# Kernel tuning notes

Hardware: AMD Instinct MI355X
Metric: run time of the kernel (lower is better)

Reference implementation:

```python
import jax, jax.numpy as jnp
import numpy as np

B, T, S, E, H = 4, 32, 256, 512, 8
D = E // H
SCALE = np.sqrt(D).astype(np.float32)
Q_MOD, K_MOD = 0, 1


def setup_inputs() -> dict:
    key = jax.random.key(0)
    ks = jax.random.split(key, 12)
    def spikes(k):
        return (jax.random.uniform(k, (B, T, S, E)) < 0.1).astype(jnp.float32)
    init = lambda k, shp: jax.random.normal(k, shp, dtype=jnp.float32) * (1.0 / np.sqrt(shp[0]))
    return {
        "query_spikes": spikes(ks[0]),
        "key_spikes": spikes(ks[1]),
        "value_spikes": spikes(ks[2]),
        "Wq": init(ks[3], (E, E)), "bq": jnp.zeros((E,), jnp.float32),
        "Wk": init(ks[4], (E, E)), "bk": jnp.zeros((E,), jnp.float32),
        "Wv": init(ks[5], (E, E)), "bv": jnp.zeros((E,), jnp.float32),
        "Wo": init(ks[6], (E, E)), "bo": jnp.zeros((E,), jnp.float32),
        "modality_weights": jnp.ones((2, H), jnp.float32),          # nn.Parameter(torch.ones(2, num_heads))
        "temporal_sync": jax.random.normal(ks[7], (T, H), jnp.float32) * 0.1,  # torch.randn(T, H) * 0.1
    }


def _spike_softmax(scores):
    # sigmoid((s - max)*5) normalized along key axis
    m = jnp.max(scores, axis=-1, keepdims=True)
    p = jax.nn.sigmoid((scores - m) * 5.0)
    return p / (jnp.sum(p, axis=-1, keepdims=True) + 1e-8)


def reference(query_spikes, key_spikes, value_spikes, Wq, bq, Wk, bk, Wv, bv, Wo, bo,
              modality_weights, temporal_sync):
    def proj(x, W, b):  # [B,T,S,E] -> [B,T,H,S,D]
        y = jnp.einsum("btse,ef->btsf", x, W) + b
        return y.reshape(B, T, S, H, D).transpose(0, 1, 3, 2, 4)

    Q = proj(query_spikes, Wq, bq)
    K = proj(key_spikes, Wk, bk)
    V = proj(value_spikes, Wv, bv)

    # attention scores across all timesteps at once: [B,T,H,Sq,Sk]
    scores = jnp.einsum("bthqd,bthkd->bthqk", Q, K) / SCALE
    mod_w = (modality_weights[Q_MOD] * modality_weights[K_MOD]).reshape(1, 1, H, 1, 1)
    scores = scores * mod_w + temporal_sync.reshape(1, T, H, 1, 1)

    attn = _spike_softmax(scores)
    attended = jnp.einsum("bthqk,bthkd->bthqd", attn, V)   # [B,T,H,Sq,D]
    attended = attended.transpose(0, 1, 3, 2, 4).reshape(B, T, S, E)
    return jnp.einsum("btse,ef->btsf", attended, Wo) + bo
```

## Files before the change

### kernel.cpp

```cpp
#include <hip/hip_runtime.h>
#include <hip/hip_bf16.h>

#define DI __device__ __forceinline__

typedef __bf16 bf16x8 __attribute__((ext_vector_type(8)));
typedef float  f32x4  __attribute__((ext_vector_type(4)));
typedef float  f32x16 __attribute__((ext_vector_type(16)));


DI ushort f2bf(float f) {
  union { float f; unsigned u; } v; v.f = f;
  unsigned r = v.u + 0x7fffu + ((v.u >> 16) & 1u);
  return (ushort)(r >> 16);
}

DI unsigned cvtpk2(float a, float b) {
  unsigned r;
  asm("v_cvt_pk_bf16_f32 %0, %1, %2" : "=v"(r) : "v"(a), "v"(b));
  return r;
}

DI float rcpf(float x) {
  float r;
  asm("v_rcp_f32 %0, %1" : "=v"(r) : "v"(x));
  return r;
}

DI void gload_lds16(const void* g, void* lds) {
  __builtin_amdgcn_global_load_lds(
      (const __attribute__((address_space(1))) unsigned*)g,
      (__attribute__((address_space(3))) unsigned*)lds, 16, 0, 0);
}

DI f32x4 zero4() { f32x4 z; z[0] = 0.f; z[1] = 0.f; z[2] = 0.f; z[3] = 0.f; return z; }

DI f32x16 zero16() {
  f32x16 z;
  for (int i = 0; i < 16; i++) z[i] = 0.f;
  return z;
}

union BF8U { ushort u[8]; unsigned d[4]; bf16x8 v; };

__global__ __launch_bounds__(256) void wtrans_kernel(
    const float* __restrict__ W0, const float* __restrict__ W1,
    const float* __restrict__ W2, const float* __restrict__ W3,
    ushort* __restrict__ out) {
  __shared__ float tile[64][65];
  const float* W = blockIdx.z == 0 ? W0 : blockIdx.z == 1 ? W1 : blockIdx.z == 2 ? W2 : W3;
  ushort* o = out + (size_t)blockIdx.z * 512 * 512;
  int k0 = blockIdx.x * 64, n0 = blockIdx.y * 64;
  int tid = threadIdx.x;
#pragma unroll
  for (int i = 0; i < 16; i++) {
    int idx = i * 256 + tid; int r = idx >> 6, c = idx & 63;
    tile[r][c] = W[(size_t)(k0 + r) * 512 + n0 + c];
  }
  __syncthreads();
#pragma unroll
  for (int i = 0; i < 16; i++) {
    int idx = i * 256 + tid; int r = idx >> 6, c = idx & 63;
    o[(size_t)(n0 + r) * 512 + k0 + c] = f2bf(tile[c][r]);
  }
}

template <int AF32>
DI void gemm_core(const void* Ap, const ushort* __restrict__ Bt, int m0, int n0,
                  char* Alds, char* Blds, f32x4 (&acc)[4][4]) {
  const float*  Af = (const float*)Ap;
  const ushort* Ah = (const ushort*)Ap;
  int tid = threadIdx.x, lane = tid & 63, wv = tid >> 6;
  int wm = (wv >> 1) * 64, wn = (wv & 1) * 64;
  int srow = tid >> 3, skg = tid & 7;

  float4 ar[8];
  bf16x8 ab[4];

  auto issueB = [&](int t) {
    char* Bb = Blds + (t & 1) * 16384;
#pragma unroll
    for (int i = 0; i < 4; i++) {
      int c = (wv * 4 + i) * 64 + lane;
      int r = c >> 3, g = (c & 7) ^ (r & 7);
      gload_lds16(Bt + (size_t)(n0 + r) * 512 + t * 64 + g * 8, Bb + (wv * 4 + i) * 1024);
    }
  };
  auto loadA = [&](int t) {
    if (AF32) {
#pragma unroll
      for (int rr = 0; rr < 4; rr++) {
        const float4* p = (const float4*)(Af + (size_t)(m0 + srow + rr * 32) * 512 + t * 64 + skg * 8);
        ar[rr * 2] = p[0]; ar[rr * 2 + 1] = p[1];
      }
    } else {
#pragma unroll
      for (int rr = 0; rr < 4; rr++)
        ab[rr] = *(const bf16x8*)(Ah + (size_t)(m0 + srow + rr * 32) * 512 + t * 64 + skg * 8);
    }
  };
  auto writeA = [&]() {
#pragma unroll
    for (int rr = 0; rr < 4; rr++) {
      int r = srow + rr * 32;
      BF8U av;
      if (AF32) {
        av.d[0] = cvtpk2(ar[rr * 2].x, ar[rr * 2].y);
        av.d[1] = cvtpk2(ar[rr * 2].z, ar[rr * 2].w);
        av.d[2] = cvtpk2(ar[rr * 2 + 1].x, ar[rr * 2 + 1].y);
        av.d[3] = cvtpk2(ar[rr * 2 + 1].z, ar[rr * 2 + 1].w);
      } else {
        av.v = ab[rr];
      }
      *(bf16x8*)(Alds + ((r * 128 + skg * 16) ^ ((r & 7) << 4))) = av.v;
    }
  };
  auto compute = [&](int t) {
    char* Bb = Blds + (t & 1) * 16384;
#pragma unroll
    for (int ks = 0; ks < 2; ks++) {
      bf16x8 a[4], b[4];
#pragma unroll
      for (int i = 0; i < 4; i++) {
        int ra = wm + i * 16 + (lane & 15);
        a[i] = *(const bf16x8*)(Alds + ((ra * 128 + (ks * 4 + (lane >> 4)) * 16) ^ ((ra & 7) << 4)));
        int rb = wn + i * 16 + (lane & 15);
        b[i] = *(const bf16x8*)(Bb + ((rb * 128 + (ks * 4 + (lane >> 4)) * 16) ^ ((rb & 7) << 4)));
      }
#pragma unroll
      for (int i = 0; i < 4; i++)
#pragma unroll
        for (int j = 0; j < 4; j++)
          acc[i][j] = __builtin_amdgcn_mfma_f32_16x16x32_bf16(a[i], b[j], acc[i][j], 0, 0, 0);
    }
  };

  issueB(0); loadA(0); writeA();
  __syncthreads();

#pragma unroll
  for (int t = 0; t < 8; t++) {
    if (t < 7) { issueB(t + 1); loadA(t + 1); }
    compute(t);
    __syncthreads();
    if (t < 7) writeA();
    __syncthreads();
  }
}

__global__ __launch_bounds__(256, 3) void qkv_gemm_kernel(
    const float* __restrict__ Aq, const float* __restrict__ Ak, const float* __restrict__ Av,
    const ushort* __restrict__ Wt, const float* __restrict__ bqp,
    const float* __restrict__ bkp, const float* __restrict__ bvp,
    ushort* __restrict__ Qw, ushort* __restrict__ Kw, ushort* __restrict__ Vt) {
  __shared__ __align__(16) char Alds[16384];
  __shared__ __align__(16) char Blds[32768];
  int z = blockIdx.z;
  const float* A = z == 0 ? Aq : z == 1 ? Ak : Av;
  const ushort* Bt = Wt + (size_t)z * 262144;
  const float* bias = z == 0 ? bqp : z == 1 ? bkp : bvp;
  int bl = ((int)blockIdx.x & 7) * 128 + ((int)blockIdx.x >> 3);
  int m0 = (bl >> 2) * 128, n0 = (bl & 3) * 128;

  f32x4 acc[4][4];
#pragma unroll
  for (int i = 0; i < 4; i++)
#pragma unroll
    for (int j = 0; j < 4; j++) acc[i][j] = zero4();

  gemm_core<1>(A, Bt, m0, n0, Alds, Blds, acc);

  int lane = threadIdx.x & 63, wv = threadIdx.x >> 6;
  int wm = (wv >> 1) * 64, wn = (wv & 1) * 64;
#pragma unroll
  for (int j = 0; j < 4; j++) {
    int col = n0 + wn + j * 16 + (lane & 15);
    float bv = bias[col];
#pragma unroll
    for (int i = 0; i < 4; i++) {
      int row0 = m0 + wm + i * 16 + (lane >> 4) * 4;
      if (z == 2) {
        int btv = row0 >> 8, s = row0 & 255;
        ushort4 w;
        w.x = f2bf(acc[i][j][0] + bv); w.y = f2bf(acc[i][j][1] + bv);
        w.z = f2bf(acc[i][j][2] + bv); w.w = f2bf(acc[i][j][3] + bv);
        *(ushort4*)(Vt + ((size_t)btv * 512 + col) * 256 + s) = w;
      } else {
        ushort* C = z == 0 ? Qw : Kw;
#pragma unroll
        for (int r = 0; r < 4; r++)
          C[(size_t)(row0 + r) * 512 + col] = f2bf(acc[i][j][r] + bv);
      }
    }
  }
}

__global__ __launch_bounds__(256, 3) void out_gemm_kernel(
    const ushort* __restrict__ A, const ushort* __restrict__ Bt,
    const float* __restrict__ bias, float* __restrict__ C) {
  __shared__ __align__(16) char Alds[16384];
  __shared__ __align__(16) char Blds[32768];
  int bl = ((int)blockIdx.x & 7) * 128 + ((int)blockIdx.x >> 3);
  int m0 = (bl >> 2) * 128, n0 = (bl & 3) * 128;

  f32x4 acc[4][4];
#pragma unroll
  for (int i = 0; i < 4; i++)
#pragma unroll
    for (int j = 0; j < 4; j++) acc[i][j] = zero4();

  gemm_core<0>(A, Bt, m0, n0, Alds, Blds, acc);

  int lane = threadIdx.x & 63, wv = threadIdx.x >> 6;
  int wm = (wv >> 1) * 64, wn = (wv & 1) * 64;
#pragma unroll
  for (int j = 0; j < 4; j++) {
    int col = n0 + wn + j * 16 + (lane & 15);
    float bv = bias[col];
#pragma unroll
    for (int i = 0; i < 4; i++) {
      int row0 = m0 + wm + i * 16 + (lane >> 4) * 4;
#pragma unroll
      for (int r = 0; r < 4; r++)
        C[(size_t)(row0 + r) * 512 + col] = acc[i][j][r] + bv;
    }
  }
}

__global__ __launch_bounds__(256) void attn_kernel(
    const ushort* __restrict__ Q, const ushort* __restrict__ K,
    const ushort* __restrict__ Vt, const float* __restrict__ mw,
    ushort* __restrict__ att) {
  __shared__ __align__(16) char Klds[32768];
  __shared__ __align__(16) char Vlds[32768];
  int tid = threadIdx.x, lane = tid & 63, wv = tid >> 6;
  int lq = lane & 31, hi = lane >> 5;
  int b = blockIdx.x;
  int h = b & 7, bt = b >> 3;
  const ushort* Qb = Q + ((size_t)bt * 256 + wv * 64) * 512 + h * 64;
  const ushort* Kb = K + ((size_t)bt * 256) * 512 + h * 64;
  const ushort* Vb = Vt + ((size_t)bt * 512 + h * 64) * 256;
  float c0 = mw[h] * mw[8 + h] * 0.125f;

#pragma unroll
  for (int i = 0; i < 8; i++) {
    int ci = (wv * 8 + i) * 64 + lane;
    int l2 = ci & 31, h2 = (ci >> 5) & 1, ds = (ci >> 6) & 3, kt = ci >> 8;
    gload_lds16(Kb + (size_t)(kt * 32 + l2) * 512 + ds * 16 + h2 * 8,
                &Klds[(wv * 8 + i) * 1024]);
  }
  bf16x8 qf[2][4];
#pragma unroll
  for (int qj = 0; qj < 2; qj++)
#pragma unroll
    for (int ds = 0; ds < 4; ds++)
      qf[qj][ds] = *(const bf16x8*)(Qb + (size_t)(qj * 32 + lq) * 512 + ds * 16 + hi * 8);
  __syncthreads();

#pragma unroll
  for (int i = 0; i < 8; i++) {
    int ci = (wv * 8 + i) * 64 + lane;
    int l2 = ci & 31, h2 = (ci >> 5) & 1, df = (ci >> 6) & 1, ks = (ci >> 7) & 1, kt = ci >> 8;
    gload_lds16(Vb + (size_t)(df * 32 + l2) * 256 + kt * 32 + ks * 16 + h2 * 8,
                &Vlds[(wv * 8 + i) * 1024]);
  }

  float mx[2] = {-3.0e38f, -3.0e38f};
#pragma unroll 2
  for (int kt = 0; kt < 8; kt++) {
    bf16x8 kf[4];
#pragma unroll
    for (int ds = 0; ds < 4; ds++)
      kf[ds] = *(const bf16x8*)(&Klds[((kt * 4 + ds) * 2 + hi) * 512 + lq * 16]);
#pragma unroll
    for (int qj = 0; qj < 2; qj++) {
      f32x16 sT = zero16();
#pragma unroll
      for (int ds = 0; ds < 4; ds++)
        sT = __builtin_amdgcn_mfma_f32_32x32x16_bf16(kf[ds], qf[qj][ds], sT, 0, 0, 0);
#pragma unroll
      for (int r = 0; r < 16; r++) mx[qj] = fmaxf(mx[qj], sT[r] * c0);
    }
  }
#pragma unroll
  for (int qj = 0; qj < 2; qj++) mx[qj] = fmaxf(mx[qj], __shfl_xor(mx[qj], 32, 64));
  __syncthreads();

  float a5 = 5.f * c0;
  float m5[2] = {5.f * mx[0], 5.f * mx[1]};
  float sm[2] = {0.f, 0.f};
  f32x16 acc[2][2];
  acc[0][0] = zero16(); acc[0][1] = zero16(); acc[1][0] = zero16(); acc[1][1] = zero16();

#pragma unroll 2
  for (int kt = 0; kt < 8; kt++) {
    bf16x8 kf[4], vf[2][2];
#pragma unroll
    for (int ds = 0; ds < 4; ds++)
      kf[ds] = *(const bf16x8*)(&Klds[((kt * 4 + ds) * 2 + hi) * 512 + lq * 16]);
#pragma unroll
    for (int ks = 0; ks < 2; ks++)
#pragma unroll
      for (int df = 0; df < 2; df++)
        vf[ks][df] = *(const bf16x8*)(&Vlds[(((kt * 2 + ks) * 2 + df) * 2 + hi) * 512 + lq * 16]);
#pragma unroll
    for (int qj = 0; qj < 2; qj++) {
      f32x16 sT = zero16();
#pragma unroll
      for (int ds = 0; ds < 4; ds++)
        sT = __builtin_amdgcn_mfma_f32_32x32x16_bf16(kf[ds], qf[qj][ds], sT, 0, 0, 0);
      unsigned pk[8];
#pragma unroll
      for (int i = 0; i < 8; i++) {
        float p0 = rcpf(1.f + __expf(m5[qj] - sT[2 * i] * a5));
        float p1 = rcpf(1.f + __expf(m5[qj] - sT[2 * i + 1] * a5));
        sm[qj] += p0 + p1;
        pk[i] = cvtpk2(p0, p1);
      }
#pragma unroll
      for (int ks = 0; ks < 2; ks++) {
        int bb = ks * 4;
        unsigned sa = (unsigned)__shfl_xor((int)pk[bb + 0], 32, 64);
        unsigned sb = (unsigned)__shfl_xor((int)pk[bb + 1], 32, 64);
        unsigned sc = (unsigned)__shfl_xor((int)pk[bb + 2], 32, 64);
        unsigned sd = (unsigned)__shfl_xor((int)pk[bb + 3], 32, 64);
        BF8U pa;
        pa.d[0] = hi ? sc : pk[bb + 0];
        pa.d[1] = hi ? sd : pk[bb + 1];
        pa.d[2] = hi ? pk[bb + 2] : sa;
        pa.d[3] = hi ? pk[bb + 3] : sb;
#pragma unroll
        for (int df = 0; df < 2; df++)
          acc[qj][df] = __builtin_amdgcn_mfma_f32_32x32x16_bf16(pa.v, vf[ks][df], acc[qj][df], 0, 0, 0);
      }
    }
  }

#pragma unroll
  for (int qj = 0; qj < 2; qj++) sm[qj] += __shfl_xor(sm[qj], 32, 64);
  float rs[2] = {rcpf(sm[0] + 1e-8f), rcpf(sm[1] + 1e-8f)};
#pragma unroll
  for (int qj = 0; qj < 2; qj++) {
#pragma unroll
    for (int r = 0; r < 16; r++) {
      int ql = (r & 3) + 8 * (r >> 2) + 4 * hi;
      float rr = __shfl(rs[qj], ql, 64);
      size_t rowbase = ((size_t)bt * 256 + wv * 64 + qj * 32 + ql) * 512 + h * 64;
#pragma unroll
      for (int df = 0; df < 2; df++)
        att[rowbase + df * 32 + lq] = f2bf(acc[qj][df][r] * rr);
    }
  }
}

extern "C" void kernel_launch(void* const* d_in, const int* in_sizes, int n_in,
                              void* d_out, int out_size, void* d_ws, size_t ws_size,
                              hipStream_t stream) {
  (void)in_sizes; (void)n_in; (void)out_size; (void)ws_size;
  const float* qs  = (const float*)d_in[0];
  const float* ksn = (const float*)d_in[1];
  const float* vsn = (const float*)d_in[2];
  const float* Wq  = (const float*)d_in[3];
  const float* bq  = (const float*)d_in[4];
  const float* Wk  = (const float*)d_in[5];
  const float* bk  = (const float*)d_in[6];
  const float* Wv  = (const float*)d_in[7];
  const float* bv  = (const float*)d_in[8];
  const float* Wo  = (const float*)d_in[9];
  const float* bo  = (const float*)d_in[10];
  const float* mw  = (const float*)d_in[11];

  char* ws = (char*)d_ws;
  ushort* Wt = (ushort*)ws;
  ushort* Qw = (ushort*)(ws + (size_t)(2u << 20));
  ushort* Kw = (ushort*)(ws + (size_t)(2u << 20) + 33554432u);
  ushort* Vt = (ushort*)(ws + (size_t)(2u << 20) + 2u * 33554432u);
  ushort* Aw = (ushort*)(ws + (size_t)(2u << 20) + 3u * 33554432u);

  wtrans_kernel<<<dim3(8, 8, 4), 256, 0, stream>>>(Wq, Wk, Wv, Wo, Wt);
  qkv_gemm_kernel<<<dim3(1024, 1, 3), 256, 0, stream>>>(qs, ksn, vsn, Wt, bq, bk, bv,
                                                        Qw, Kw, Vt);
  attn_kernel<<<dim3(1024), 256, 0, stream>>>(Qw, Kw, Vt, mw, Aw);
  out_gemm_kernel<<<dim3(1024), 256, 0, stream>>>(Aw, Wt + 3 * 262144, bo, (float*)d_out);
}
```

Measured before the change: 212.2 us.

## Pre-convert spike inputs to bf16 and use async LDS-load pipelined GEMM

Adds a separate kernel that converts the fp32 spike inputs to bf16 in workspace, so both GEMMs can load A tiles directly into LDS with global_load_lds. The GEMM core becomes a double-buffered, prefetch-two-ahead pipeline with explicit vmcnt waits and barriers. This is meant to remove register staging and conversion from the GEMM inner loop. It adds an extra full read/write pass over the inputs and doubles LDS use, which lowers occupancy to two blocks per CU.

```diff
diff --git a/kernel.cpp b/kernel.cpp
--- a/kernel.cpp
+++ b/kernel.cpp
@@ -31,6 +31,11 @@
       (const __attribute__((address_space(1))) unsigned*)g,
       (__attribute__((address_space(3))) unsigned*)lds, 16, 0, 0);
 }
+
+#define WAITVM8   asm volatile("s_waitcnt vmcnt(8)" ::: "memory")
+#define WAITVM0   asm volatile("s_waitcnt vmcnt(0)" ::: "memory")
+#define WAITLGKM0 asm volatile("s_waitcnt lgkmcnt(0)" ::: "memory")
+#define SBAR      __builtin_amdgcn_s_barrier()
 
 DI f32x4 zero4() { f32x4 z; z[0] = 0.f; z[1] = 0.f; z[2] = 0.f; z[3] = 0.f; return z; }
 
@@ -64,57 +69,39 @@
   }
 }
 
-template <int AF32>
-DI void gemm_core(const void* Ap, const ushort* __restrict__ Bt, int m0, int n0,
-                  char* Alds, char* Blds, f32x4 (&acc)[4][4]) {
-  const float*  Af = (const float*)Ap;
-  const ushort* Ah = (const ushort*)Ap;
+__global__ __launch_bounds__(256) void cvt_kernel(
+    const float* __restrict__ q, const float* __restrict__ k,
+    const float* __restrict__ v, uint4* __restrict__ o) {
+  const float* src = blockIdx.y == 0 ? q : blockIdx.y == 1 ? k : v;
+  uint4* dst = o + (size_t)blockIdx.y * 2097152;
+  for (int i = blockIdx.x * 256 + threadIdx.x; i < 2097152; i += 2048 * 256) {
+    const float4* p = (const float4*)(src + (size_t)i * 8);
+    float4 a = p[0], b = p[1];
+    uint4 w;
+    w.x = cvtpk2(a.x, a.y); w.y = cvtpk2(a.z, a.w);
+    w.z = cvtpk2(b.x, b.y); w.w = cvtpk2(b.z, b.w);
+    dst[i] = w;
+  }
+}
+
+DI void gemm_core(const ushort* __restrict__ A, const ushort* __restrict__ Bt,
+                  int m0, int n0, char* Alds, char* Blds, f32x4 (&acc)[4][4]) {
   int tid = threadIdx.x, lane = tid & 63, wv = tid >> 6;
   int wm = (wv >> 1) * 64, wn = (wv & 1) * 64;
-  int srow = tid >> 3, skg = tid & 7;
-
-  float4 ar[8];
-  bf16x8 ab[4];
-
-  auto issueB = [&](int t) {
+
+  auto stage = [&](int t) {
+    char* Ab = Alds + (t & 1) * 16384;
     char* Bb = Blds + (t & 1) * 16384;
 #pragma unroll
     for (int i = 0; i < 4; i++) {
       int c = (wv * 4 + i) * 64 + lane;
       int r = c >> 3, g = (c & 7) ^ (r & 7);
+      gload_lds16(A + (size_t)(m0 + r) * 512 + t * 64 + g * 8, Ab + (wv * 4 + i) * 1024);
       gload_lds16(Bt + (size_t)(n0 + r) * 512 + t * 64 + g * 8, Bb + (wv * 4 + i) * 1024);
-    }
-  };
-  auto loadA = [&](int t) {
-    if (AF32) {
-#pragma unroll
-      for (int rr = 0; rr < 4; rr++) {
-        const float4* p = (const float4*)(Af + (size_t)(m0 + srow + rr * 32) * 512 + t * 64 + skg * 8);
-        ar[rr * 2] = p[0]; ar[rr * 2 + 1] = p[1];
-      }
-    } else {
-#pragma unroll
-      for (int rr = 0; rr < 4; rr++)
-        ab[rr] = *(const bf16x8*)(Ah + (size_t)(m0 + srow + rr * 32) * 512 + t * 64 + skg * 8);
-    }
-  };
-  auto writeA = [&]() {
-#pragma unroll
-    for (int rr = 0; rr < 4; rr++) {
-      int r = srow + rr * 32;
-      BF8U av;
-      if (AF32) {
-        av.d[0] = cvtpk2(ar[rr * 2].x, ar[rr * 2].y);
-        av.d[1] = cvtpk2(ar[rr * 2].z, ar[rr * 2].w);
-        av.d[2] = cvtpk2(ar[rr * 2 + 1].x, ar[rr * 2 + 1].y);
-        av.d[3] = cvtpk2(ar[rr * 2 + 1].z, ar[rr * 2 + 1].w);
-      } else {
-        av.v = ab[rr];
-      }
-      *(bf16x8*)(Alds + ((r * 128 + skg * 16) ^ ((r & 7) << 4))) = av.v;
     }
   };
   auto compute = [&](int t) {
+    char* Ab = Alds + (t & 1) * 16384;
     char* Bb = Blds + (t & 1) * 16384;
 #pragma unroll
     for (int ks = 0; ks < 2; ks++) {
@@ -122,7 +109,7 @@
 #pragma unroll
       for (int i = 0; i < 4; i++) {
         int ra = wm + i * 16 + (lane & 15);
-        a[i] = *(const bf16x8*)(Alds + ((ra * 128 + (ks * 4 + (lane >> 4)) * 16) ^ ((ra & 7) << 4)));
+        a[i] = *(const bf16x8*)(Ab + ((ra * 128 + (ks * 4 + (lane >> 4)) * 16) ^ ((ra & 7) << 4)));
         int rb = wn + i * 16 + (lane & 15);
         b[i] = *(const bf16x8*)(Bb + ((rb * 128 + (ks * 4 + (lane >> 4)) * 16) ^ ((rb & 7) << 4)));
       }
@@ -134,28 +121,28 @@
     }
   };
 
-  issueB(0); loadA(0); writeA();
-  __syncthreads();
-
+  stage(0);
+  stage(1);
 #pragma unroll
   for (int t = 0; t < 8; t++) {
-    if (t < 7) { issueB(t + 1); loadA(t + 1); }
+    if (t < 7) WAITVM8; else WAITVM0;
+    SBAR;
     compute(t);
-    __syncthreads();
-    if (t < 7) writeA();
-    __syncthreads();
-  }
-}
-
-__global__ __launch_bounds__(256, 3) void qkv_gemm_kernel(
-    const float* __restrict__ Aq, const float* __restrict__ Ak, const float* __restrict__ Av,
-    const ushort* __restrict__ Wt, const float* __restrict__ bqp,
-    const float* __restrict__ bkp, const float* __restrict__ bvp,
+    WAITLGKM0;
+    SBAR;
+    if (t < 6) stage(t + 2);
+  }
+}
+
+__global__ __launch_bounds__(256, 2) void qkv_gemm_kernel(
+    const ushort* __restrict__ Asp, const ushort* __restrict__ Wt,
+    const float* __restrict__ bqp, const float* __restrict__ bkp,
+    const float* __restrict__ bvp,
     ushort* __restrict__ Qw, ushort* __restrict__ Kw, ushort* __restrict__ Vt) {
-  __shared__ __align__(16) char Alds[16384];
+  __shared__ __align__(16) char Alds[32768];
   __shared__ __align__(16) char Blds[32768];
   int z = blockIdx.z;
-  const float* A = z == 0 ? Aq : z == 1 ? Ak : Av;
+  const ushort* A = Asp + (size_t)z * 16777216;
   const ushort* Bt = Wt + (size_t)z * 262144;
   const float* bias = z == 0 ? bqp : z == 1 ? bkp : bvp;
   int bl = ((int)blockIdx.x & 7) * 128 + ((int)blockIdx.x >> 3);
@@ -167,7 +154,7 @@
 #pragma unroll
     for (int j = 0; j < 4; j++) acc[i][j] = zero4();
 
-  gemm_core<1>(A, Bt, m0, n0, Alds, Blds, acc);
+  gemm_core(A, Bt, m0, n0, Alds, Blds, acc);
 
   int lane = threadIdx.x & 63, wv = threadIdx.x >> 6;
   int wm = (wv >> 1) * 64, wn = (wv & 1) * 64;
@@ -194,10 +181,10 @@
   }
 }
 
-__global__ __launch_bounds__(256, 3) void out_gemm_kernel(
+__global__ __launch_bounds__(256, 2) void out_gemm_kernel(
     const ushort* __restrict__ A, const ushort* __restrict__ Bt,
     const float* __restrict__ bias, float* __restrict__ C) {
-  __shared__ __align__(16) char Alds[16384];
+  __shared__ __align__(16) char Alds[32768];
   __shared__ __align__(16) char Blds[32768];
   int bl = ((int)blockIdx.x & 7) * 128 + ((int)blockIdx.x >> 3);
   int m0 = (bl >> 2) * 128, n0 = (bl & 3) * 128;
@@ -208,7 +195,7 @@
 #pragma unroll
     for (int j = 0; j < 4; j++) acc[i][j] = zero4();
 
-  gemm_core<0>(A, Bt, m0, n0, Alds, Blds, acc);
+  gemm_core(A, Bt, m0, n0, Alds, Blds, acc);
 
   int lane = threadIdx.x & 63, wv = threadIdx.x >> 6;
   int wm = (wv >> 1) * 64, wn = (wv & 1) * 64;
@@ -370,15 +357,18 @@
   const float* mw  = (const float*)d_in[11];
 
   char* ws = (char*)d_ws;
-  ushort* Wt = (ushort*)ws;
-  ushort* Qw = (ushort*)(ws + (size_t)(2u << 20));
-  ushort* Kw = (ushort*)(ws + (size_t)(2u << 20) + 33554432u);
-  ushort* Vt = (ushort*)(ws + (size_t)(2u << 20) + 2u * 33554432u);
-  ushort* Aw = (ushort*)(ws + (size_t)(2u << 20) + 3u * 33554432u);
+  const size_t SLOT = 33554432u;
+  ushort* Wt  = (ushort*)ws;
+  char*   s0  = ws + (size_t)(2u << 20);
+  ushort* Qw  = (ushort*)(s0 + 0 * SLOT);
+  ushort* Kw  = (ushort*)(s0 + 1 * SLOT);
+  ushort* Vt  = (ushort*)(s0 + 2 * SLOT);
+  ushort* Asp = (ushort*)(s0 + 3 * SLOT);
+  ushort* Aw  = (ushort*)(s0 + 3 * SLOT);
 
   wtrans_kernel<<<dim3(8, 8, 4), 256, 0, stream>>>(Wq, Wk, Wv, Wo, Wt);
-  qkv_gemm_kernel<<<dim3(1024, 1, 3), 256, 0, stream>>>(qs, ksn, vsn, Wt, bq, bk, bv,
-                                                        Qw, Kw, Vt);
+  cvt_kernel<<<dim3(2048, 3), 256, 0, stream>>>(qs, ksn, vsn, (uint4*)Asp);
+  qkv_gemm_kernel<<<dim3(1024, 1, 3), 256, 0, stream>>>(Asp, Wt, bq, bk, bv, Qw, Kw, Vt);
   attn_kernel<<<dim3(1024), 256, 0, stream>>>(Qw, Kw, Vt, mw, Aw);
   out_gemm_kernel<<<dim3(1024), 256, 0, stream>>>(Aw, Wt + 3 * 262144, bo, (float*)d_out);
 }
```

Measured after the change: 236.4 us. 1.11x slower.

## Deepen GEMM software pipeline with double-buffered A and explicit waitcnt barriers

Applied to the files above, without the earlier changes.

Replaces the shared gemm_core with two specialised GEMM kernels. Each uses double-buffered A and B tiles in LDS, prefetches two k-steps ahead, and uses explicit s_waitcnt vmcnt/lgkmcnt with raw s_barrier, which cuts the two full __syncthreads per iteration down to finer-grained waits. The output GEMM now loads its bf16 A operand straight into LDS with global_load_lds instead of going through registers. LDS per block grows to 64KB and launch bounds drop from 3 to 2 blocks per CU, trading occupancy for deeper overlap; the hand-counted vmcnt values are fragile if the number of loads changes.

```diff
diff --git a/kernel.cpp b/kernel.cpp
--- a/kernel.cpp
+++ b/kernel.cpp
@@ -31,6 +31,12 @@
       (const __attribute__((address_space(1))) unsigned*)g,
       (__attribute__((address_space(3))) unsigned*)lds, 16, 0, 0);
 }
+
+#define WAITVM12  asm volatile("s_waitcnt vmcnt(12)" ::: "memory")
+#define WAITVM8   asm volatile("s_waitcnt vmcnt(8)" ::: "memory")
+#define WAITVM0   asm volatile("s_waitcnt vmcnt(0)" ::: "memory")
+#define WAITLGKM0 asm volatile("s_waitcnt lgkmcnt(0)" ::: "memory")
+#define SBAR      __builtin_amdgcn_s_barrier()
 
 DI f32x4 zero4() { f32x4 z; z[0] = 0.f; z[1] = 0.f; z[2] = 0.f; z[3] = 0.f; return z; }
 
@@ -64,18 +70,51 @@
   }
 }
 
-template <int AF32>
-DI void gemm_core(const void* Ap, const ushort* __restrict__ Bt, int m0, int n0,
-                  char* Alds, char* Blds, f32x4 (&acc)[4][4]) {
-  const float*  Af = (const float*)Ap;
-  const ushort* Ah = (const ushort*)Ap;
+__global__ __launch_bounds__(256, 2) void qkv_gemm_kernel(
+    const float* __restrict__ Aq, const float* __restrict__ Ak, const float* __restrict__ Av,
+    const ushort* __restrict__ Wt, const float* __restrict__ bqp,
+    const float* __restrict__ bkp, const float* __restrict__ bvp,
+    ushort* __restrict__ Qw, ushort* __restrict__ Kw, ushort* __restrict__ Vt) {
+  __shared__ __align__(16) char Alds[32768];
+  __shared__ __align__(16) char Blds[32768];
+  int z = blockIdx.z;
+  const float* Af = z == 0 ? Aq : z == 1 ? Ak : Av;
+  const ushort* Bt = Wt + (size_t)z * 262144;
+  const float* bias = z == 0 ? bqp : z == 1 ? bkp : bvp;
+  int bl = ((int)blockIdx.x & 7) * 128 + ((int)blockIdx.x >> 3);
+  int m0 = (bl >> 2) * 128, n0 = (bl & 3) * 128;
   int tid = threadIdx.x, lane = tid & 63, wv = tid >> 6;
   int wm = (wv >> 1) * 64, wn = (wv & 1) * 64;
   int srow = tid >> 3, skg = tid & 7;
 
+  f32x4 acc[4][4];
+#pragma unroll
+  for (int i = 0; i < 4; i++)
+#pragma unroll
+    for (int j = 0; j < 4; j++) acc[i][j] = zero4();
+
   float4 ar[8];
-  bf16x8 ab[4];
-
+
+  auto loadA = [&](int t) {
+#pragma unroll
+    for (int rr = 0; rr < 4; rr++) {
+      const float4* p = (const float4*)(Af + (size_t)(m0 + srow + rr * 32) * 512 + t * 64 + skg * 8);
+      ar[rr * 2] = p[0]; ar[rr * 2 + 1] = p[1];
+    }
+  };
+  auto writeA = [&](int t) {
+    char* Ab = Alds + (t & 1) * 16384;
+#pragma unroll
+    for (int rr = 0; rr < 4; rr++) {
+      int r = srow + rr * 32;
+      BF8U av;
+      av.d[0] = cvtpk2(ar[rr * 2].x, ar[rr * 2].y);
+      av.d[1] = cvtpk2(ar[rr * 2].z, ar[rr * 2].w);
+      av.d[2] = cvtpk2(ar[rr * 2 + 1].x, ar[rr * 2 + 1].y);
+      av.d[3] = cvtpk2(ar[rr * 2 + 1].z, ar[rr * 2 + 1].w);
+      *(bf16x8*)(Ab + ((r * 128 + skg * 16) ^ ((r & 7) << 4))) = av.v;
+    }
+  };
   auto issueB = [&](int t) {
     char* Bb = Blds + (t & 1) * 16384;
 #pragma unroll
@@ -85,36 +124,8 @@
       gload_lds16(Bt + (size_t)(n0 + r) * 512 + t * 64 + g * 8, Bb + (wv * 4 + i) * 1024);
     }
   };
-  auto loadA = [&](int t) {
-    if (AF32) {
-#pragma unroll
-      for (int rr = 0; rr < 4; rr++) {
-        const float4* p = (const float4*)(Af + (size_t)(m0 + srow + rr * 32) * 512 + t * 64 + skg * 8);
-        ar[rr * 2] = p[0]; ar[rr * 2 + 1] = p[1];
-      }
-    } else {
-#pragma unroll
-      for (int rr = 0; rr < 4; rr++)
-        ab[rr] = *(const bf16x8*)(Ah + (size_t)(m0 + srow + rr * 32) * 512 + t * 64 + skg * 8);
-    }
-  };
-  auto writeA = [&]() {
-#pragma unroll
-    for (int rr = 0; rr < 4; rr++) {
-      int r = srow + rr * 32;
-      BF8U av;
-      if (AF32) {
-        av.d[0] = cvtpk2(ar[rr * 2].x, ar[rr * 2].y);
-        av.d[1] = cvtpk2(ar[rr * 2].z, ar[rr * 2].w);
-        av.d[2] = cvtpk2(ar[rr * 2 + 1].x, ar[rr * 2 + 1].y);
-        av.d[3] = cvtpk2(ar[rr * 2 + 1].z, ar[rr * 2 + 1].w);
-      } else {
-        av.v = ab[rr];
-      }
-      *(bf16x8*)(Alds + ((r * 128 + skg * 16) ^ ((r & 7) << 4))) = av.v;
-    }
-  };
   auto compute = [&](int t) {
+    char* Ab = Alds + (t & 1) * 16384;
     char* Bb = Blds + (t & 1) * 16384;
 #pragma unroll
     for (int ks = 0; ks < 2; ks++) {
@@ -122,7 +133,7 @@
 #pragma unroll
       for (int i = 0; i < 4; i++) {
         int ra = wm + i * 16 + (lane & 15);
-        a[i] = *(const bf16x8*)(Alds + ((ra * 128 + (ks * 4 + (lane >> 4)) * 16) ^ ((ra & 7) << 4)));
+        a[i] = *(const bf16x8*)(Ab + ((ra * 128 + (ks * 4 + (lane >> 4)) * 16) ^ ((ra & 7) << 4)));
         int rb = wn + i * 16 + (lane & 15);
         b[i] = *(const bf16x8*)(Bb + ((rb * 128 + (ks * 4 + (lane >> 4)) * 16) ^ ((rb & 7) << 4)));
       }
@@ -134,43 +145,24 @@
     }
   };
 
-  issueB(0); loadA(0); writeA();
-  __syncthreads();
+  loadA(0); issueB(0);
+  WAITVM0;
+  writeA(0);
+  loadA(1); issueB(1);
+  WAITLGKM0;
 
 #pragma unroll
   for (int t = 0; t < 8; t++) {
-    if (t < 7) { issueB(t + 1); loadA(t + 1); }
+    if (t >= 1) { if (t < 7) WAITVM12; else WAITVM0; }
+    SBAR;
     compute(t);
-    __syncthreads();
-    if (t < 7) writeA();
-    __syncthreads();
-  }
-}
-
-__global__ __launch_bounds__(256, 3) void qkv_gemm_kernel(
-    const float* __restrict__ Aq, const float* __restrict__ Ak, const float* __restrict__ Av,
-    const ushort* __restrict__ Wt, const float* __restrict__ bqp,
-    const float* __restrict__ bkp, const float* __restrict__ bvp,
-    ushort* __restrict__ Qw, ushort* __restrict__ Kw, ushort* __restrict__ Vt) {
-  __shared__ __align__(16) char Alds[16384];
-  __shared__ __align__(16) char Blds[32768];
-  int z = blockIdx.z;
-  const float* A = z == 0 ? Aq : z == 1 ? Ak : Av;
-  const ushort* Bt = Wt + (size_t)z * 262144;
-  const float* bias = z == 0 ? bqp : z == 1 ? bkp : bvp;
-  int bl = ((int)blockIdx.x & 7) * 128 + ((int)blockIdx.x >> 3);
-  int m0 = (bl >> 2) * 128, n0 = (bl & 3) * 128;
-
-  f32x4 acc[4][4];
-#pragma unroll
-  for (int i = 0; i < 4; i++)
-#pragma unroll
-    for (int j = 0; j < 4; j++) acc[i][j] = zero4();
-
-  gemm_core<1>(A, Bt, m0, n0, Alds, Blds, acc);
-
-  int lane = threadIdx.x & 63, wv = threadIdx.x >> 6;
-  int wm = (wv >> 1) * 64, wn = (wv & 1) * 64;
+    if (t < 7) writeA(t + 1);
+    if (t < 6) loadA(t + 2);
+    WAITLGKM0;
+    SBAR;
+    if (t < 6) issueB(t + 2);
+  }
+
 #pragma unroll
   for (int j = 0; j < 4; j++) {
     int col = n0 + wn + j * 16 + (lane & 15);
@@ -194,13 +186,15 @@
   }
 }
 
-__global__ __launch_bounds__(256, 3) void out_gemm_kernel(
+__global__ __launch_bounds__(256, 2) void out_gemm_kernel(
     const ushort* __restrict__ A, const ushort* __restrict__ Bt,
     const float* __restrict__ bias, float* __restrict__ C) {
-  __shared__ __align__(16) char Alds[16384];
+  __shared__ __align__(16) char Alds[32768];
   __shared__ __align__(16) char Blds[32768];
   int bl = ((int)blockIdx.x & 7) * 128 + ((int)blockIdx.x >> 3);
   int m0 = (bl >> 2) * 128, n0 = (bl & 3) * 128;
+  int tid = threadIdx.x, lane = tid & 63, wv = tid >> 6;
+  int wm = (wv >> 1) * 64, wn = (wv & 1) * 64;
 
   f32x4 acc[4][4];
 #pragma unroll
@@ -208,17 +202,58 @@
 #pragma unroll
     for (int j = 0; j < 4; j++) acc[i][j] = zero4();
 
-  gemm_core<0>(A, Bt, m0, n0, Alds, Blds, acc);
-
-  int lane = threadIdx.x & 63, wv = threadIdx.x >> 6;
-  int wm = (wv >> 1) * 64, wn = (wv & 1) * 64;
+  auto stage = [&](int t) {
+    char* Ab = Alds + (t & 1) * 16384;
+    char* Bb = Blds + (t & 1) * 16384;
+#pragma unroll
+    for (int i = 0; i < 4; i++) {
+      int c = (wv * 4 + i) * 64 + lane;
+      int r = c >> 3, g = (c & 7) ^ (r & 7);
+      gload_lds16(A + (size_t)(m0 + r) * 512 + t * 64 + g * 8, Ab + (wv * 4 + i) * 1024);
+      gload_lds16(Bt + (size_t)(n0 + r) * 512 + t * 64 + g * 8, Bb + (wv * 4 + i) * 1024);
+    }
+  };
+  auto compute = [&](int t) {
+    char* Ab = Alds + (t & 1) * 16384;
+    char* Bb = Blds + (t & 1) * 16384;
+#pragma unroll
+    for (int ks = 0; ks < 2; ks++) {
+      bf16x8 a[4], b[4];
+#pragma unroll
+      for (int i = 0; i < 4; i++) {
+        int ra = wm + i * 16 + (lane & 15);
+        a[i] = *(const bf16x8*)(Ab + ((ra * 128 + (ks * 4 + (lane >> 4)) * 16) ^ ((ra & 7) << 4)));
+        int rb = wn + i * 16 + (lane & 15);
+        b[i] = *(const bf16x8*)(Bb + ((rb * 128 + (ks * 4 + (lane >> 4)) * 16) ^ ((rb & 7) << 4)));
+      }
+#pragma unroll
+      for (int i = 0; i < 4; i++)
+#pragma unroll
+        for (int j = 0; j < 4; j++)
+          acc[i][j] = __builtin_amdgcn_mfma_f32_16x16x32_bf16(a[i], b[j], acc[i][j], 0, 0, 0);
+    }
+  };
+
+  stage(0);
+  stage(1);
+#pragma unroll
+  for (int t = 0; t < 8; t++) {
+    if (t < 7) { WAITVM8; } else { WAITVM0; }
+    SBAR;
+    compute(t);
+    WAITLGKM0;
+    SBAR;
+    if (t < 6) stage(t + 2);
+  }
+
+  int lane2 = threadIdx.x & 63;
 #pragma unroll
   for (int j = 0; j < 4; j++) {
-    int col = n0 + wn + j * 16 + (lane & 15);
+    int col = n0 + wn + j * 16 + (lane2 & 15);
     float bv = bias[col];
 #pragma unroll
     for (int i = 0; i < 4; i++) {
-      int row0 = m0 + wm + i * 16 + (lane >> 4) * 4;
+      int row0 = m0 + wm + i * 16 + (lane2 >> 4) * 4;
 #pragma unroll
       for (int r = 0; r < 4; r++)
         C[(size_t)(row0 + r) * 512 + col] = acc[i][j][r] + bv;
@@ -370,11 +405,13 @@
   const float* mw  = (const float*)d_in[11];
 
   char* ws = (char*)d_ws;
+  const size_t SLOT = 33554432u;
   ushort* Wt = (ushort*)ws;
-  ushort* Qw = (ushort*)(ws + (size_t)(2u << 20));
-  ushort* Kw = (ushort*)(ws + (size_t)(2u << 20) + 33554432u);
-  ushort* Vt = (ushort*)(ws + (size_t)(2u << 20) + 2u * 33554432u);
-  ushort* Aw = (ushort*)(ws + (size_t)(2u << 20) + 3u * 33554432u);
+  char*   s0 = ws + (size_t)(2u << 20);
+  ushort* Qw = (ushort*)(s0 + 0 * SLOT);
+  ushort* Kw = (ushort*)(s0 + 1 * SLOT);
+  ushort* Vt = (ushort*)(s0 + 2 * SLOT);
+  ushort* Aw = (ushort*)(s0 + 3 * SLOT);
 
   wtrans_kernel<<<dim3(8, 8, 4), 256, 0, stream>>>(Wq, Wk, Wv, Wo, Wt);
   qkv_gemm_kernel<<<dim3(1024, 1, 3), 256, 0, stream>>>(qs, ksn, vsn, Wt, bq, bk, bv,
```

New measurement: 214.5 us. Within noise of the previous version (+1.1%).
